# Optimization experiments

Measured on AMD Instinct MI355X. Metric: run time of the kernel, lower is better.

Reference implementation:

```python
import jax, jax.numpy as jnp
import numpy as np

N_NODES = 50000
N_EDGES = 800000
IN_DIM = 128
HIDDEN = 64      # out_channels per head (concat=False -> head mean)
HEADS = 2
N_GRAPHS = 64
LN_EPS = 1e-5


def _layer_norm(x, g, b):
    mu = jnp.mean(x, axis=-1, keepdims=True)
    var = jnp.mean((x - mu) ** 2, axis=-1, keepdims=True)
    return (x - mu) * jax.lax.rsqrt(var + LN_EPS) * g + b


def _transformer_conv(x, src, dst, Wq, bq, Wk, bk, Wv, bv, Ws, bs):
    # PyG TransformerConv, concat=False, root_weight=True, beta=False.
    n = x.shape[0]
    q = (x @ Wq + bq).reshape(n, HEADS, -1)[dst]   # [E, H, D] query at target i
    k = (x @ Wk + bk).reshape(n, HEADS, -1)[src]   # [E, H, D] key at source j
    v = (x @ Wv + bv).reshape(n, HEADS, -1)[src]   # [E, H, D] value at source j
    d = q.shape[-1]
    score = jnp.sum(q * k, axis=-1) / jnp.sqrt(jnp.asarray(d, x.dtype))  # [E, H]
    # segment softmax over incoming edges of each target node
    smax = jax.ops.segment_max(score, dst, num_segments=n)
    e = jnp.exp(score - smax[dst])
    denom = jax.ops.segment_sum(e, dst, num_segments=n)
    alpha = e / denom[dst]                                              # [E, H]
    agg = jax.ops.segment_sum(alpha[..., None] * v, dst, num_segments=n)  # [N, H, D]
    out = jnp.mean(agg, axis=1)                     # concat=False -> head mean
    return out + x @ Ws + bs                        # root/skip connection


def setup_inputs() -> dict:
    key = jax.random.key(0)
    ks = jax.random.split(key, 40)
    inp = {}
    inp["x"] = jax.random.normal(ks[0], (N_NODES, IN_DIM), jnp.float32)
    inp["edge_index"] = jax.random.randint(ks[1], (2, N_EDGES), 0, N_NODES, dtype=jnp.int64)
    inp["batch"] = jnp.sort(jax.random.randint(ks[2], (N_NODES,), 0, N_GRAPHS, dtype=jnp.int64))
    dims = [(IN_DIM, HIDDEN), (HIDDEN, HIDDEN), (HIDDEN, HIDDEN)]
    i = 3
    for l, (din, dout) in enumerate(dims):
        for nm in ("q", "k", "v"):
            inp[f"W{nm}{l}"] = jax.random.normal(ks[i], (din, HEADS * dout), jnp.float32) * 0.05; i += 1
            inp[f"b{nm}{l}"] = jnp.zeros((HEADS * dout,), jnp.float32)
        inp[f"Ws{l}"] = jax.random.normal(ks[i], (din, dout), jnp.float32) * 0.05; i += 1
        inp[f"bs{l}"] = jnp.zeros((dout,), jnp.float32)
    for l in range(2):  # LayerNorm after layers 0 and 1 only
        inp[f"g{l}"] = jnp.ones((HIDDEN,), jnp.float32)
        inp[f"beta{l}"] = jnp.zeros((HIDDEN,), jnp.float32)
    inp["Wp"] = jax.random.normal(ks[i], (HIDDEN, 1), jnp.float32) * 0.05
    inp["bp"] = jnp.zeros((1,), jnp.float32)
    return inp


def reference(x, edge_index, batch,
              Wq0, bq0, Wk0, bk0, Wv0, bv0, Ws0, bs0,
              Wq1, bq1, Wk1, bk1, Wv1, bv1, Ws1, bs1,
              Wq2, bq2, Wk2, bk2, Wv2, bv2, Ws2, bs2,
              g0, beta0, g1, beta1, Wp, bp):
    src, dst = edge_index[0], edge_index[1]
    layers = [(Wq0, bq0, Wk0, bk0, Wv0, bv0, Ws0, bs0),
              (Wq1, bq1, Wk1, bk1, Wv1, bv1, Ws1, bs1),
              (Wq2, bq2, Wk2, bk2, Wv2, bv2, Ws2, bs2)]
    lns = [(g0, beta0), (g1, beta1)]
    h = x
    for i, p in enumerate(layers):
        h = _transformer_conv(h, src, dst, *p)
        h = jax.nn.relu(h)  # dropout p=0.0 / eval -> identity
        if i != len(layers) - 1:
            h = _layer_norm(h, *lns[i])
    # global mean pool per graph
    cnt = jax.ops.segment_sum(jnp.ones((h.shape[0],), h.dtype), batch, num_segments=N_GRAPHS)
    pooled = jax.ops.segment_sum(h, batch, num_segments=N_GRAPHS) / jnp.maximum(cnt, 1.0)[:, None]
    return pooled @ Wp + bp
```

## Files before the change

### kernel.cpp

```cpp
#include <hip/hip_runtime.h>
#include <hip/hip_fp16.h>
#include <math.h>

#define HIDDEN 64
#define HEADS 2
#define NCOLS 448
#define QS_COLS 192
#define KV_COLS 256
#define N_GRAPHS 64
#define LN_EPS 1e-5f

typedef _Float16 half8 __attribute__((ext_vector_type(8)));
typedef float    f32x4 __attribute__((ext_vector_type(4)));


__global__ void cast_f2h_kernel(const float* __restrict__ in, _Float16* __restrict__ out, int n4)
{
    int i = blockIdx.x * 256 + threadIdx.x;
    if (i < n4) {
        float4 v = *(const float4*)&in[i * 4];
        __half2 a = __floats2half2_rn(v.x, v.y);
        __half2 b = __floats2half2_rn(v.z, v.w);
        uint2 pk;
        pk.x = *(unsigned int*)&a;
        pk.y = *(unsigned int*)&b;
        *(uint2*)&out[i * 4] = pk;
    }
}

__global__ void pack_kernel(const float* __restrict__ Wq, const float* __restrict__ Wk,
                            const float* __restrict__ Wv, const float* __restrict__ Ws,
                            const float* __restrict__ bq, const float* __restrict__ bk,
                            const float* __restrict__ bv, const float* __restrict__ bs,
                            _Float16* __restrict__ Bt, float* __restrict__ bcat, int K)
{
    int idx = blockIdx.x * 256 + threadIdx.x;
    int total = NCOLS * K;
    if (idx < total) {
        int c = idx / K, k = idx - c * K;
        float v;
        if      (c < 128) v = Wq[k * 128 + c] * 0.125f;
        else if (c < 256) v = Wk[k * 128 + (c - 128)];
        else if (c < 384) v = Wv[k * 128 + (c - 256)];
        else              v = Ws[k * 64  + (c - 384)];
        Bt[idx] = (_Float16)v;
    }
    if (idx < NCOLS) {
        float b;
        if      (idx < 128) b = bq[idx] * 0.125f;
        else if (idx < 256) b = bk[idx - 128];
        else if (idx < 384) b = bv[idx - 256];
        else                b = bs[idx - 384];
        bcat[idx] = b;
    }
}

template<int K, int NT>
__device__ __forceinline__ void gemm_body(
    const _Float16* __restrict__ Ah, const float* __restrict__ bias,
    float* __restrict__ qs, __half* __restrict__ kvh,
    const _Float16* Bs, int M, int colBase, int chunkRow0, int tid)
{
    int lane = tid & 63;
    int w    = tid >> 6;
    int fr   = lane & 15;
    int g    = lane >> 4;
    int row0 = chunkRow0 + w * 16;
    int arow = row0 + fr;
    if (arow > M - 1) arow = M - 1;

    f32x4 acc[NT];
    #pragma unroll
    for (int c = 0; c < NT; ++c) acc[c] = (f32x4){0.f, 0.f, 0.f, 0.f};

    #pragma unroll
    for (int ks = 0; ks < K / 32; ++ks) {
        int k0 = ks * 32 + g * 8;
        half8 af = *(const half8*)&Ah[(size_t)arow * K + k0];
        #pragma unroll
        for (int c = 0; c < NT; ++c) {
            int rl   = c * 16 + fr;
            int byte = rl * (K * 2) + k0 * 2;
            int sw   = byte ^ ((rl & 7) << 4);
            half8 bf = *(const half8*)((const char*)Bs + sw);
            acc[c] = __builtin_amdgcn_mfma_f32_16x16x32_f16(af, bf, acc[c], 0, 0, 0);
        }
    }

    #pragma unroll
    for (int c = 0; c < NT; ++c) {
        int col = colBase + c * 16 + fr;
        float bs = bias[col];
        #pragma unroll
        for (int j = 0; j < 4; ++j) {
            int row = row0 + g * 4 + j;
            if (row >= M) continue;
            float o = acc[c][j] + bs;
            if (col < 128) {
                qs[(size_t)row * QS_COLS + col] = o;
            } else if (col >= 384) {
                qs[(size_t)row * QS_COLS + 128 + (col - 384)] = o;
            } else {
                int cc  = col - 128;
                int mat = cc >> 7;
                int hh  = (cc >> 6) & 1;
                int d   = cc & 63;
                int pos = mat * 128 + (d >> 2) * 8 + hh * 4 + (d & 3);
                kvh[(size_t)row * KV_COLS + pos] = __float2half_rn(o);
            }
        }
    }
}

template<int K>
__global__ __launch_bounds__(512, 4) void gemm_mfma_kernel(
    const _Float16* __restrict__ Ah,
    const _Float16* __restrict__ Bt,
    const float* __restrict__ bias,
    float* __restrict__ qs, __half* __restrict__ kvh, int M)
{
    __shared__ _Float16 Bs[256 * K];

    int tid    = threadIdx.x;
    int colblk = blockIdx.x & 1;
    int chunk  = blockIdx.x >> 1;
    int colBase = colblk ? 256 : 0;
    int cols    = colblk ? 192 : 256;

    int bytes = cols * K * 2;
    const char* src = (const char*)Bt + (size_t)colBase * K * 2;
    for (int i = tid * 16; i < bytes; i += 512 * 16) {
        int rl = i / (K * 2);
        int sw = i ^ ((rl & 7) << 4);
        *(half8*)((char*)Bs + sw) = *(const half8*)(src + i);
    }
    __syncthreads();

    if (colblk == 0)
        gemm_body<K, 16>(Ah, bias, qs, kvh, Bs, M, 0,   chunk * 128, tid);
    else
        gemm_body<K, 12>(Ah, bias, qs, kvh, Bs, M, 256, chunk * 128, tid);
}

__global__ void hist_kernel(const int* __restrict__ dst, int* __restrict__ counts, int E)
{
    int i = blockIdx.x * 256 + threadIdx.x;
    if (i < E) atomicAdd(&counts[dst[i]], 1);
}

__global__ __launch_bounds__(256) void block_reduce_kernel(
    const int* __restrict__ counts, int* __restrict__ bsum, int N)
{
    __shared__ int s[256];
    int t = threadIdx.x;
    int i = blockIdx.x * 256 + t;
    s[t] = (i < N) ? counts[i] : 0;
    __syncthreads();
    #pragma unroll
    for (int o = 128; o; o >>= 1) {
        if (t < o) s[t] += s[t + o];
        __syncthreads();
    }
    if (t == 0) bsum[blockIdx.x] = s[0];
}

__global__ __launch_bounds__(256) void scan_partials_kernel(
    const int* __restrict__ bsum, int* __restrict__ boff, int nb, int* __restrict__ rowN)
{
    __shared__ int s[256];
    int t = threadIdx.x;
    int v = (t < nb) ? bsum[t] : 0;
    s[t] = v;
    __syncthreads();
    #pragma unroll
    for (int o = 1; o < 256; o <<= 1) {
        int x = (t >= o) ? s[t - o] : 0;
        __syncthreads();
        s[t] += x;
        __syncthreads();
    }
    if (t < nb) boff[t] = s[t] - v;
    if (t == nb - 1) rowN[0] = s[t];
}

__global__ __launch_bounds__(256) void block_scan_kernel(
    const int* __restrict__ counts, const int* __restrict__ boff,
    int* __restrict__ row_ptr, int* __restrict__ cursor, int N)
{
    __shared__ int s[256];
    int t = threadIdx.x;
    int i = blockIdx.x * 256 + t;
    int v = (i < N) ? counts[i] : 0;
    s[t] = v;
    __syncthreads();
    #pragma unroll
    for (int o = 1; o < 256; o <<= 1) {
        int x = (t >= o) ? s[t - o] : 0;
        __syncthreads();
        s[t] += x;
        __syncthreads();
    }
    if (i < N) {
        int excl = s[t] - v + boff[blockIdx.x];
        row_ptr[i] = excl;
        cursor[i]  = excl;
    }
}

__global__ void scatter_kernel(const int* __restrict__ ei, int* __restrict__ cursor,
                               int* __restrict__ src_sorted, int E)
{
    int i = blockIdx.x * 256 + threadIdx.x;
    if (i < E) {
        int d = ei[E + i];
        int pos = atomicAdd(&cursor[d], 1);
        src_sorted[pos] = ei[i];
    }
}

__device__ __forceinline__ float dpp_sum16(float x)
{
    float t;
    t = __int_as_float(__builtin_amdgcn_mov_dpp(__float_as_int(x), 0xB1,  0xF, 0xF, true)); x += t;
    t = __int_as_float(__builtin_amdgcn_mov_dpp(__float_as_int(x), 0x4E,  0xF, 0xF, true)); x += t;
    t = __int_as_float(__builtin_amdgcn_mov_dpp(__float_as_int(x), 0x141, 0xF, 0xF, true)); x += t;
    t = __int_as_float(__builtin_amdgcn_mov_dpp(__float_as_int(x), 0x140, 0xF, 0xF, true)); x += t;
    return x;
}

__global__ __launch_bounds__(256) void edge_conv_kernel(
    const float* __restrict__ qs, const __half* __restrict__ kvh,
    const int* __restrict__ row_ptr, const int* __restrict__ src_sorted,
    const float* __restrict__ gamma, const float* __restrict__ beta,
    float* __restrict__ hout, _Float16* __restrict__ hh, int N, int do_ln)
{
    int wave = threadIdx.x >> 6;
    int lane = threadIdx.x & 63;
    int g    = lane >> 4;
    int sub  = lane & 15;
    int node = blockIdx.x * 4 + wave;
    if (node >= N) return;

    const float* qb = qs + (size_t)node * QS_COLS;
    float4 q0 = *(const float4*)&qb[sub * 4];
    float4 q1 = *(const float4*)&qb[64 + sub * 4];

    int e0 = row_ptr[node], e1 = row_ptr[node + 1];
    int deg = e1 - e0;

    float  m0 = -1e30f, m1 = -1e30f;
    float  s0 = 0.f, s1 = 0.f;
    float4 a0 = make_float4(0.f, 0.f, 0.f, 0.f);
    float4 a1 = make_float4(0.f, 0.f, 0.f, 0.f);

    int  e    = e0 + g;
    bool have = (e < e1);
    uint4 kraw, vraw;
    if (have) {
        int j = src_sorted[e];
        const __half* jb = kvh + (size_t)j * KV_COLS;
        kraw = *(const uint4*)&jb[sub * 8];
        vraw = *(const uint4*)&jb[128 + sub * 8];
    }

    while (have) {
        int  en    = e + 4;
        bool haven = (en < e1);
        uint4 krn, vrn;
        if (haven) {
            int jn = src_sorted[en];
            const __half* jbn = kvh + (size_t)jn * KV_COLS;
            krn = *(const uint4*)&jbn[sub * 8];
            vrn = *(const uint4*)&jbn[128 + sub * 8];
        }

        const __half2* kp = (const __half2*)&kraw;
        float2 ka = __half22float2(kp[0]), kb = __half22float2(kp[1]);
        float2 kc = __half22float2(kp[2]), kd = __half22float2(kp[3]);

        float p0 = fmaf(q0.w, kb.y, fmaf(q0.z, kb.x, fmaf(q0.y, ka.y, q0.x * ka.x)));
        float p1 = fmaf(q1.w, kd.y, fmaf(q1.z, kd.x, fmaf(q1.y, kc.y, q1.x * kc.x)));
        float sc0 = dpp_sum16(p0);
        float sc1 = dpp_sum16(p1);

        const __half2* vp = (const __half2*)&vraw;
        float2 va = __half22float2(vp[0]), vb = __half22float2(vp[1]);
        float2 vc = __half22float2(vp[2]), vd = __half22float2(vp[3]);

        float nm0 = fmaxf(m0, sc0);
        float f0  = __expf(m0 - nm0);
        float w0  = __expf(sc0 - nm0);
        s0 = fmaf(s0, f0, w0);
        a0.x = fmaf(a0.x, f0, w0 * va.x);
        a0.y = fmaf(a0.y, f0, w0 * va.y);
        a0.z = fmaf(a0.z, f0, w0 * vb.x);
        a0.w = fmaf(a0.w, f0, w0 * vb.y);
        m0 = nm0;

        float nm1 = fmaxf(m1, sc1);
        float f1  = __expf(m1 - nm1);
        float w1  = __expf(sc1 - nm1);
        s1 = fmaf(s1, f1, w1);
        a1.x = fmaf(a1.x, f1, w1 * vc.x);
        a1.y = fmaf(a1.y, f1, w1 * vc.y);
        a1.z = fmaf(a1.z, f1, w1 * vd.x);
        a1.w = fmaf(a1.w, f1, w1 * vd.y);
        m1 = nm1;

        kraw = krn; vraw = vrn; e = en; have = haven;
    }

    #pragma unroll
    for (int offm = 16; offm <= 32; offm <<= 1) {
        float mo0 = __shfl_xor(m0, offm);
        float so0 = __shfl_xor(s0, offm);
        float4 ao0;
        ao0.x = __shfl_xor(a0.x, offm); ao0.y = __shfl_xor(a0.y, offm);
        ao0.z = __shfl_xor(a0.z, offm); ao0.w = __shfl_xor(a0.w, offm);
        float nm = fmaxf(m0, mo0);
        float fa = __expf(m0 - nm), fb = __expf(mo0 - nm);
        s0 = s0 * fa + so0 * fb;
        a0.x = a0.x * fa + ao0.x * fb; a0.y = a0.y * fa + ao0.y * fb;
        a0.z = a0.z * fa + ao0.z * fb; a0.w = a0.w * fa + ao0.w * fb;
        m0 = nm;

        float mo1 = __shfl_xor(m1, offm);
        float so1 = __shfl_xor(s1, offm);
        float4 ao1;
        ao1.x = __shfl_xor(a1.x, offm); ao1.y = __shfl_xor(a1.y, offm);
        ao1.z = __shfl_xor(a1.z, offm); ao1.w = __shfl_xor(a1.w, offm);
        nm = fmaxf(m1, mo1);
        fa = __expf(m1 - nm); fb = __expf(mo1 - nm);
        s1 = s1 * fa + so1 * fb;
        a1.x = a1.x * fa + ao1.x * fb; a1.y = a1.y * fa + ao1.y * fb;
        a1.z = a1.z * fa + ao1.z * fb; a1.w = a1.w * fa + ao1.w * fb;
        m1 = nm;
    }

    float4 skip = *(const float4*)&qb[128 + sub * 4];
    float4 o;
    if (deg > 0) {
        float r0 = 0.5f / s0, r1 = 0.5f / s1;
        o.x = a0.x * r0 + a1.x * r1 + skip.x;
        o.y = a0.y * r0 + a1.y * r1 + skip.y;
        o.z = a0.z * r0 + a1.z * r1 + skip.z;
        o.w = a0.w * r0 + a1.w * r1 + skip.w;
    } else {
        o = skip;
    }
    o.x = fmaxf(o.x, 0.f); o.y = fmaxf(o.y, 0.f);
    o.z = fmaxf(o.z, 0.f); o.w = fmaxf(o.w, 0.f);

    if (do_ln) {
        float mu = dpp_sum16(o.x + o.y + o.z + o.w) * (1.0f / 64.0f);
        float dx = o.x - mu, dy = o.y - mu, dz = o.z - mu, dw = o.w - mu;
        float var = dpp_sum16(dx * dx + dy * dy + dz * dz + dw * dw) * (1.0f / 64.0f);
        float rs = rsqrtf(var + LN_EPS);
        float4 gm = *(const float4*)&gamma[sub * 4];
        float4 bt = *(const float4*)&beta[sub * 4];
        o.x = dx * rs * gm.x + bt.x;
        o.y = dy * rs * gm.y + bt.y;
        o.z = dz * rs * gm.z + bt.z;
        o.w = dw * rs * gm.w + bt.w;
    }
    if (g == 0) {
        *(float4*)&hout[(size_t)node * HIDDEN + sub * 4] = o;
        __half2 h01 = __floats2half2_rn(o.x, o.y);
        __half2 h23 = __floats2half2_rn(o.z, o.w);
        uint2 pk;
        pk.x = *(unsigned int*)&h01;
        pk.y = *(unsigned int*)&h23;
        *(uint2*)&hh[(size_t)node * HIDDEN + sub * 4] = pk;
    }
}

#define POOL_CHUNK 32
__global__ __launch_bounds__(64) void pool_kernel(const float* __restrict__ h,
                                                  const int* __restrict__ batch,
                                                  float* __restrict__ pooled,
                                                  float* __restrict__ cnt, int N)
{
    int lane = threadIdx.x;
    int start = blockIdx.x * POOL_CHUNK;
    if (start >= N) return;
    int end = min(start + POOL_CHUNK, N);
    int b0 = batch[start];
    int b1 = batch[end - 1];

    if (b0 == b1) {
        float acc = 0.f;
        #pragma unroll 4
        for (int i = start; i < end; ++i)
            acc += h[(size_t)i * HIDDEN + lane];
        atomicAdd(&pooled[b0 * HIDDEN + lane], acc);
        if (lane == 0) atomicAdd(&cnt[b0], (float)(end - start));
    } else {
        float acc = 0.f;
        int cur = b0, c = 0;
        for (int i = start; i < end; ++i) {
            int b = batch[i];
            if (b != cur) {
                atomicAdd(&pooled[cur * HIDDEN + lane], acc);
                if (lane == 0) atomicAdd(&cnt[cur], (float)c);
                acc = 0.f; c = 0; cur = b;
            }
            acc += h[(size_t)i * HIDDEN + lane];
            ++c;
        }
        atomicAdd(&pooled[cur * HIDDEN + lane], acc);
        if (lane == 0) atomicAdd(&cnt[cur], (float)c);
    }
}

__global__ void final_kernel(const float* __restrict__ pooled, const float* __restrict__ cnt,
                             const float* __restrict__ Wp, const float* __restrict__ bp,
                             float* __restrict__ out)
{
    int g = threadIdx.x;
    float c = fmaxf(cnt[g], 1.0f);
    float s = 0.f;
    for (int d = 0; d < HIDDEN; ++d) s += pooled[g * HIDDEN + d] * Wp[d];
    out[g] = s / c + bp[0];
}

extern "C" void kernel_launch(void* const* d_in, const int* in_sizes, int n_in,
                              void* d_out, int out_size, void* d_ws, size_t ws_size,
                              hipStream_t stream)
{
    const float* x    = (const float*)d_in[0];
    const int*   ei   = (const int*)d_in[1];
    const int*   batch= (const int*)d_in[2];

    const float* Wl[3][4];
    const float* bl[3][4];
    for (int l = 0; l < 3; ++l) {
        int b = 3 + l * 8;
        Wl[l][0] = (const float*)d_in[b + 0]; bl[l][0] = (const float*)d_in[b + 1];
        Wl[l][1] = (const float*)d_in[b + 2]; bl[l][1] = (const float*)d_in[b + 3];
        Wl[l][2] = (const float*)d_in[b + 4]; bl[l][2] = (const float*)d_in[b + 5];
        Wl[l][3] = (const float*)d_in[b + 6]; bl[l][3] = (const float*)d_in[b + 7];
    }
    const float* g0    = (const float*)d_in[27];
    const float* beta0 = (const float*)d_in[28];
    const float* g1    = (const float*)d_in[29];
    const float* beta1 = (const float*)d_in[30];
    const float* Wp    = (const float*)d_in[31];
    const float* bp    = (const float*)d_in[32];

    const int N = in_sizes[0] / 128;
    const int E = in_sizes[1] / 2;

    size_t off = 0;
    auto carve = [&](size_t bytes) -> char* {
        char* p = (char*)d_ws + off;
        off = (off + bytes + 255) & ~(size_t)255;
        return p;
    };
    float*     qs     = (float*)carve((size_t)N * QS_COLS * 4);
    __half*    kvh    = (__half*)carve((size_t)N * KV_COLS * 2);
    float*     h      = (float*)carve((size_t)N * HIDDEN * 4);
    _Float16*  hh     = (_Float16*)carve((size_t)N * HIDDEN * 2);
    _Float16*  xh     = (_Float16*)carve((size_t)N * 128 * 2);
    _Float16*  Bt     = (_Float16*)carve((size_t)NCOLS * 128 * 2);
    float*     bcat   = (float*)carve(NCOLS * 4);
    int*       counts = (int*)carve((size_t)N * 4);
    int*       row_ptr= (int*)carve((size_t)(N + 1) * 4);
    int*       cursor = (int*)carve((size_t)N * 4);
    int*       src_sorted = (int*)carve((size_t)E * 4);
    int*       bsum   = (int*)carve(1024 * 4);
    int*       boff   = (int*)carve(1024 * 4);
    float*     pooled = (float*)carve((size_t)(N_GRAPHS * HIDDEN + N_GRAPHS) * 4);
    float*     cntf   = pooled + N_GRAPHS * HIDDEN;

    const int nb = (N + 255) / 256;

    hipMemsetAsync(counts, 0, (size_t)N * 4, stream);
    hist_kernel<<<(E + 255) / 256, 256, 0, stream>>>(ei + E, counts, E);
    block_reduce_kernel<<<nb, 256, 0, stream>>>(counts, bsum, N);
    scan_partials_kernel<<<1, 256, 0, stream>>>(bsum, boff, nb, &row_ptr[N]);
    block_scan_kernel<<<nb, 256, 0, stream>>>(counts, boff, row_ptr, cursor, N);
    scatter_kernel<<<(E + 255) / 256, 256, 0, stream>>>(ei, cursor, src_sorted, E);

    {
        int n4 = (N * 128) / 4;
        cast_f2h_kernel<<<(n4 + 255) / 256, 256, 0, stream>>>(x, xh, n4);
    }

    const int gemm_grid = 2 * ((N + 127) / 128);

    for (int l = 0; l < 3; ++l) {
        int K = (l == 0) ? 128 : 64;
        int packTot = NCOLS * K;
        pack_kernel<<<(packTot + 255) / 256, 256, 0, stream>>>(
            Wl[l][0], Wl[l][1], Wl[l][2], Wl[l][3],
            bl[l][0], bl[l][1], bl[l][2], bl[l][3], Bt, bcat, K);
        if (l == 0)
            gemm_mfma_kernel<128><<<gemm_grid, 512, 0, stream>>>(xh, Bt, bcat, qs, kvh, N);
        else
            gemm_mfma_kernel<64><<<gemm_grid, 512, 0, stream>>>(hh, Bt, bcat, qs, kvh, N);
        int do_ln = (l < 2) ? 1 : 0;
        const float* gg = (l == 0) ? g0 : g1;
        const float* bb = (l == 0) ? beta0 : beta1;
        edge_conv_kernel<<<(N + 3) / 4, 256, 0, stream>>>(
            qs, kvh, row_ptr, src_sorted, gg, bb, h, hh, N, do_ln);
    }

    hipMemsetAsync(pooled, 0, (size_t)(N_GRAPHS * HIDDEN + N_GRAPHS) * 4, stream);
    pool_kernel<<<(N + POOL_CHUNK - 1) / POOL_CHUNK, 64, 0, stream>>>(h, batch, pooled, cntf, N);
    final_kernel<<<1, 64, 0, stream>>>(pooled, cntf, Wp, bp, (float*)d_out);
}
```

Baseline: 415.3 us.

## Process eight edges per wave with 8-lane groups and plain K/V layout

```diff
diff --git a/kernel.cpp b/kernel.cpp
--- a/kernel.cpp
+++ b/kernel.cpp
@@ -9,10 +9,10 @@
 #define KV_COLS 256
 #define N_GRAPHS 64
 #define LN_EPS 1e-5f
+#define Q_SCALE 0.18033688011112042f
 
 typedef _Float16 half8 __attribute__((ext_vector_type(8)));
 typedef float    f32x4 __attribute__((ext_vector_type(4)));
-
 
 __global__ void cast_f2h_kernel(const float* __restrict__ in, _Float16* __restrict__ out, int n4)
 {
@@ -39,7 +39,7 @@
     if (idx < total) {
         int c = idx / K, k = idx - c * K;
         float v;
-        if      (c < 128) v = Wq[k * 128 + c] * 0.125f;
+        if      (c < 128) v = Wq[k * 128 + c] * Q_SCALE;
         else if (c < 256) v = Wk[k * 128 + (c - 128)];
         else if (c < 384) v = Wv[k * 128 + (c - 256)];
         else              v = Ws[k * 64  + (c - 384)];
@@ -47,7 +47,7 @@
     }
     if (idx < NCOLS) {
         float b;
-        if      (idx < 128) b = bq[idx] * 0.125f;
+        if      (idx < 128) b = bq[idx] * Q_SCALE;
         else if (idx < 256) b = bk[idx - 128];
         else if (idx < 384) b = bv[idx - 256];
         else                b = bs[idx - 384];
@@ -101,12 +101,7 @@
             } else if (col >= 384) {
                 qs[(size_t)row * QS_COLS + 128 + (col - 384)] = o;
             } else {
-                int cc  = col - 128;
-                int mat = cc >> 7;
-                int hh  = (cc >> 6) & 1;
-                int d   = cc & 63;
-                int pos = mat * 128 + (d >> 2) * 8 + hh * 4 + (d & 3);
-                kvh[(size_t)row * KV_COLS + pos] = __float2half_rn(o);
+                kvh[(size_t)row * KV_COLS + (col - 128)] = __float2half_rn(o);
             }
         }
     }
@@ -218,13 +213,12 @@
     }
 }
 
-__device__ __forceinline__ float dpp_sum16(float x)
+__device__ __forceinline__ float dpp_sum8(float x)
 {
     float t;
     t = __int_as_float(__builtin_amdgcn_mov_dpp(__float_as_int(x), 0xB1,  0xF, 0xF, true)); x += t;
     t = __int_as_float(__builtin_amdgcn_mov_dpp(__float_as_int(x), 0x4E,  0xF, 0xF, true)); x += t;
     t = __int_as_float(__builtin_amdgcn_mov_dpp(__float_as_int(x), 0x141, 0xF, 0xF, true)); x += t;
-    t = __int_as_float(__builtin_amdgcn_mov_dpp(__float_as_int(x), 0x140, 0xF, 0xF, true)); x += t;
     return x;
 }
 
@@ -236,141 +230,168 @@
 {
     int wave = threadIdx.x >> 6;
     int lane = threadIdx.x & 63;
-    int g    = lane >> 4;
-    int sub  = lane & 15;
+    int g    = lane >> 3;
+    int sub  = lane & 7;
     int node = blockIdx.x * 4 + wave;
     if (node >= N) return;
 
     const float* qb = qs + (size_t)node * QS_COLS;
-    float4 q0 = *(const float4*)&qb[sub * 4];
-    float4 q1 = *(const float4*)&qb[64 + sub * 4];
+    float q0r[8], q1r[8];
+    {
+        float4 a = *(const float4*)&qb[sub * 8];
+        float4 b = *(const float4*)&qb[sub * 8 + 4];
+        float4 c = *(const float4*)&qb[64 + sub * 8];
+        float4 d = *(const float4*)&qb[64 + sub * 8 + 4];
+        q0r[0]=a.x; q0r[1]=a.y; q0r[2]=a.z; q0r[3]=a.w;
+        q0r[4]=b.x; q0r[5]=b.y; q0r[6]=b.z; q0r[7]=b.w;
+        q1r[0]=c.x; q1r[1]=c.y; q1r[2]=c.z; q1r[3]=c.w;
+        q1r[4]=d.x; q1r[5]=d.y; q1r[6]=d.z; q1r[7]=d.w;
+    }
 
     int e0 = row_ptr[node], e1 = row_ptr[node + 1];
     int deg = e1 - e0;
 
-    float  m0 = -1e30f, m1 = -1e30f;
-    float  s0 = 0.f, s1 = 0.f;
-    float4 a0 = make_float4(0.f, 0.f, 0.f, 0.f);
-    float4 a1 = make_float4(0.f, 0.f, 0.f, 0.f);
+    float m0 = -1e30f, m1 = -1e30f, s0 = 0.f, s1 = 0.f;
+    float a0[8] = {}, a1[8] = {};
 
     int  e    = e0 + g;
     bool have = (e < e1);
-    uint4 kraw, vraw;
+    uint4 k0r, k1r, v0r, v1r;
     if (have) {
-        int j = src_sorted[e];
-        const __half* jb = kvh + (size_t)j * KV_COLS;
-        kraw = *(const uint4*)&jb[sub * 8];
-        vraw = *(const uint4*)&jb[128 + sub * 8];
+        const __half* jb = kvh + (size_t)src_sorted[e] * KV_COLS;
+        k0r = *(const uint4*)&jb[sub * 8];
+        k1r = *(const uint4*)&jb[64 + sub * 8];
+        v0r = *(const uint4*)&jb[128 + sub * 8];
+        v1r = *(const uint4*)&jb[192 + sub * 8];
     }
 
     while (have) {
-        int  en    = e + 4;
+        int  en    = e + 8;
         bool haven = (en < e1);
-        uint4 krn, vrn;
+        uint4 k0n, k1n, v0n, v1n;
         if (haven) {
-            int jn = src_sorted[en];
-            const __half* jbn = kvh + (size_t)jn * KV_COLS;
-            krn = *(const uint4*)&jbn[sub * 8];
-            vrn = *(const uint4*)&jbn[128 + sub * 8];
-        }
-
-        const __half2* kp = (const __half2*)&kraw;
-        float2 ka = __half22float2(kp[0]), kb = __half22float2(kp[1]);
-        float2 kc = __half22float2(kp[2]), kd = __half22float2(kp[3]);
-
-        float p0 = fmaf(q0.w, kb.y, fmaf(q0.z, kb.x, fmaf(q0.y, ka.y, q0.x * ka.x)));
-        float p1 = fmaf(q1.w, kd.y, fmaf(q1.z, kd.x, fmaf(q1.y, kc.y, q1.x * kc.x)));
-        float sc0 = dpp_sum16(p0);
-        float sc1 = dpp_sum16(p1);
-
-        const __half2* vp = (const __half2*)&vraw;
-        float2 va = __half22float2(vp[0]), vb = __half22float2(vp[1]);
-        float2 vc = __half22float2(vp[2]), vd = __half22float2(vp[3]);
+            const __half* jbn = kvh + (size_t)src_sorted[en] * KV_COLS;
+            k0n = *(const uint4*)&jbn[sub * 8];
+            k1n = *(const uint4*)&jbn[64 + sub * 8];
+            v0n = *(const uint4*)&jbn[128 + sub * 8];
+            v1n = *(const uint4*)&jbn[192 + sub * 8];
+        }
+
+        const __half* k0h = (const __half*)&k0r;
+        const __half* k1h = (const __half*)&k1r;
+        float p0 = 0.f, p1 = 0.f;
+        #pragma unroll
+        for (int i = 0; i < 8; ++i) {
+            p0 = fmaf(q0r[i], __half2float(k0h[i]), p0);
+            p1 = fmaf(q1r[i], __half2float(k1h[i]), p1);
+        }
+        float sc0 = dpp_sum8(p0);
+        float sc1 = dpp_sum8(p1);
+
+        const __half* v0h = (const __half*)&v0r;
+        const __half* v1h = (const __half*)&v1r;
 
         float nm0 = fmaxf(m0, sc0);
-        float f0  = __expf(m0 - nm0);
-        float w0  = __expf(sc0 - nm0);
+        float f0  = exp2f(m0 - nm0);
+        float w0  = exp2f(sc0 - nm0);
         s0 = fmaf(s0, f0, w0);
-        a0.x = fmaf(a0.x, f0, w0 * va.x);
-        a0.y = fmaf(a0.y, f0, w0 * va.y);
-        a0.z = fmaf(a0.z, f0, w0 * vb.x);
-        a0.w = fmaf(a0.w, f0, w0 * vb.y);
+        #pragma unroll
+        for (int i = 0; i < 8; ++i)
+            a0[i] = fmaf(a0[i], f0, w0 * __half2float(v0h[i]));
         m0 = nm0;
 
         float nm1 = fmaxf(m1, sc1);
-        float f1  = __expf(m1 - nm1);
-        float w1  = __expf(sc1 - nm1);
+        float f1  = exp2f(m1 - nm1);
+        float w1  = exp2f(sc1 - nm1);
         s1 = fmaf(s1, f1, w1);
-        a1.x = fmaf(a1.x, f1, w1 * vc.x);
-        a1.y = fmaf(a1.y, f1, w1 * vc.y);
-        a1.z = fmaf(a1.z, f1, w1 * vd.x);
-        a1.w = fmaf(a1.w, f1, w1 * vd.y);
+        #pragma unroll
+        for (int i = 0; i < 8; ++i)
+            a1[i] = fmaf(a1[i], f1, w1 * __half2float(v1h[i]));
         m1 = nm1;
 
-        kraw = krn; vraw = vrn; e = en; have = haven;
-    }
-
-    #pragma unroll
-    for (int offm = 16; offm <= 32; offm <<= 1) {
+        k0r = k0n; k1r = k1n; v0r = v0n; v1r = v1n;
+        e = en; have = haven;
+    }
+
+    #pragma unroll
+    for (int offm = 8; offm <= 32; offm <<= 1) {
         float mo0 = __shfl_xor(m0, offm);
         float so0 = __shfl_xor(s0, offm);
-        float4 ao0;
-        ao0.x = __shfl_xor(a0.x, offm); ao0.y = __shfl_xor(a0.y, offm);
-        ao0.z = __shfl_xor(a0.z, offm); ao0.w = __shfl_xor(a0.w, offm);
-        float nm = fmaxf(m0, mo0);
-        float fa = __expf(m0 - nm), fb = __expf(mo0 - nm);
+        float nm  = fmaxf(m0, mo0);
+        float fa  = exp2f(m0 - nm), fb = exp2f(mo0 - nm);
         s0 = s0 * fa + so0 * fb;
-        a0.x = a0.x * fa + ao0.x * fb; a0.y = a0.y * fa + ao0.y * fb;
-        a0.z = a0.z * fa + ao0.z * fb; a0.w = a0.w * fa + ao0.w * fb;
+        #pragma unroll
+        for (int i = 0; i < 8; ++i) {
+            float ao = __shfl_xor(a0[i], offm);
+            a0[i] = a0[i] * fa + ao * fb;
+        }
         m0 = nm;
 
         float mo1 = __shfl_xor(m1, offm);
         float so1 = __shfl_xor(s1, offm);
-        float4 ao1;
-        ao1.x = __shfl_xor(a1.x, offm); ao1.y = __shfl_xor(a1.y, offm);
-        ao1.z = __shfl_xor(a1.z, offm); ao1.w = __shfl_xor(a1.w, offm);
         nm = fmaxf(m1, mo1);
-        fa = __expf(m1 - nm); fb = __expf(mo1 - nm);
+        fa = exp2f(m1 - nm); fb = exp2f(mo1 - nm);
         s1 = s1 * fa + so1 * fb;
-        a1.x = a1.x * fa + ao1.x * fb; a1.y = a1.y * fa + ao1.y * fb;
-        a1.z = a1.z * fa + ao1.z * fb; a1.w = a1.w * fa + ao1.w * fb;
+        #pragma unroll
+        for (int i = 0; i < 8; ++i) {
+            float ao = __shfl_xor(a1[i], offm);
+            a1[i] = a1[i] * fa + ao * fb;
+        }
         m1 = nm;
     }
 
-    float4 skip = *(const float4*)&qb[128 + sub * 4];
-    float4 o;
-    if (deg > 0) {
-        float r0 = 0.5f / s0, r1 = 0.5f / s1;
-        o.x = a0.x * r0 + a1.x * r1 + skip.x;
-        o.y = a0.y * r0 + a1.y * r1 + skip.y;
-        o.z = a0.z * r0 + a1.z * r1 + skip.z;
-        o.w = a0.w * r0 + a1.w * r1 + skip.w;
-    } else {
-        o = skip;
-    }
-    o.x = fmaxf(o.x, 0.f); o.y = fmaxf(o.y, 0.f);
-    o.z = fmaxf(o.z, 0.f); o.w = fmaxf(o.w, 0.f);
+    float o[8];
+    {
+        float4 ska = *(const float4*)&qb[128 + sub * 8];
+        float4 skb = *(const float4*)&qb[128 + sub * 8 + 4];
+        float sk[8] = {ska.x, ska.y, ska.z, ska.w, skb.x, skb.y, skb.z, skb.w};
+        if (deg > 0) {
+            float r0 = 0.5f / s0, r1 = 0.5f / s1;
+            #pragma unroll
+            for (int i = 0; i < 8; ++i)
+                o[i] = fmaxf(a0[i] * r0 + a1[i] * r1 + sk[i], 0.f);
+        } else {
+            #pragma unroll
+            for (int i = 0; i < 8; ++i) o[i] = fmaxf(sk[i], 0.f);
+        }
+    }
 
     if (do_ln) {
-        float mu = dpp_sum16(o.x + o.y + o.z + o.w) * (1.0f / 64.0f);
-        float dx = o.x - mu, dy = o.y - mu, dz = o.z - mu, dw = o.w - mu;
-        float var = dpp_sum16(dx * dx + dy * dy + dz * dz + dw * dw) * (1.0f / 64.0f);
+        float loc = 0.f;
+        #pragma unroll
+        for (int i = 0; i < 8; ++i) loc += o[i];
+        float mu = dpp_sum8(loc) * (1.0f / 64.0f);
+        float lv = 0.f;
+        float d[8];
+        #pragma unroll
+        for (int i = 0; i < 8; ++i) { d[i] = o[i] - mu; lv = fmaf(d[i], d[i], lv); }
+        float var = dpp_sum8(lv) * (1.0f / 64.0f);
         float rs = rsqrtf(var + LN_EPS);
-        float4 gm = *(const float4*)&gamma[sub * 4];
-        float4 bt = *(const float4*)&beta[sub * 4];
-        o.x = dx * rs * gm.x + bt.x;
-        o.y = dy * rs * gm.y + bt.y;
-        o.z = dz * rs * gm.z + bt.z;
-        o.w = dw * rs * gm.w + bt.w;
-    }
+        float4 gma = *(const float4*)&gamma[sub * 8];
+        float4 gmb = *(const float4*)&gamma[sub * 8 + 4];
+        float4 bta = *(const float4*)&beta[sub * 8];
+        float4 btb = *(const float4*)&beta[sub * 8 + 4];
+        float gm[8] = {gma.x, gma.y, gma.z, gma.w, gmb.x, gmb.y, gmb.z, gmb.w};
+        float bt[8] = {bta.x, bta.y, bta.z, bta.w, btb.x, btb.y, btb.z, btb.w};
+        #pragma unroll
+        for (int i = 0; i < 8; ++i) o[i] = d[i] * rs * gm[i] + bt[i];
+    }
+
     if (g == 0) {
-        *(float4*)&hout[(size_t)node * HIDDEN + sub * 4] = o;
-        __half2 h01 = __floats2half2_rn(o.x, o.y);
-        __half2 h23 = __floats2half2_rn(o.z, o.w);
-        uint2 pk;
+        float4 oa = make_float4(o[0], o[1], o[2], o[3]);
+        float4 ob = make_float4(o[4], o[5], o[6], o[7]);
+        *(float4*)&hout[(size_t)node * HIDDEN + sub * 8]     = oa;
+        *(float4*)&hout[(size_t)node * HIDDEN + sub * 8 + 4] = ob;
+        __half2 h01 = __floats2half2_rn(o[0], o[1]);
+        __half2 h23 = __floats2half2_rn(o[2], o[3]);
+        __half2 h45 = __floats2half2_rn(o[4], o[5]);
+        __half2 h67 = __floats2half2_rn(o[6], o[7]);
+        uint4 pk;
         pk.x = *(unsigned int*)&h01;
         pk.y = *(unsigned int*)&h23;
-        *(uint2*)&hh[(size_t)node * HIDDEN + sub * 4] = pk;
+        pk.z = *(unsigned int*)&h45;
+        pk.w = *(unsigned int*)&h67;
+        *(uint4*)&hh[(size_t)node * HIDDEN + sub * 8] = pk;
     }
 }
 
```

Result: no change. 423.5 us (+2.0%).
